# Kernel optimization log

Hardware: AMD Instinct MI355X
Metric: run time of the kernel (lower is better)

## Reference

```python
import jax, jax.numpy as jnp
import numpy as np

B, N, M, D = 4, 512, 512, 128
H, DOUT = 256, 128

def setup_inputs() -> dict:
    key = jax.random.key(0)
    k = jax.random.split(key, 4)
    X = jax.random.normal(k[0], (B, N, D), dtype=jnp.float32)
    Y = jax.random.normal(k[1], (B, M, D), dtype=jnp.float32)
    W1 = jax.random.normal(k[2], (2 * D, H), dtype=jnp.float32) / np.sqrt(2 * D)
    b1 = jnp.zeros((H,), dtype=jnp.float32)
    W2 = jax.random.normal(k[3], (H, DOUT), dtype=jnp.float32) / np.sqrt(H)
    b2 = jnp.zeros((DOUT,), dtype=jnp.float32)
    return {"X": X, "Y": Y, "W1": W1, "b1": b1, "W2": W2, "b2": b2}

def reference(X, Y, W1, b1, W2, b2):
    # pairs[b,n,m,:] = concat(Y[b,m], X[b,n])  -> [B,N,M,2D]
    n_ = X.shape[1]
    m_ = Y.shape[1]
    Ye = jnp.broadcast_to(Y[:, None, :, :], (X.shape[0], n_, m_, Y.shape[-1]))
    Xe = jnp.broadcast_to(X[:, :, None, :], (X.shape[0], n_, m_, X.shape[-1]))
    pairs = jnp.concatenate([Ye, Xe], axis=-1)
    # pointwise MLP: Linear -> ReLU -> Linear
    hdn = jax.nn.relu(jnp.einsum('bnmd,dh->bnmh', pairs, W1) + b1)
    Z = jnp.einsum('bnmh,ho->bnmo', hdn, W2) + b2
    # pool='sum' over the M (neighbor) dimension
    return jnp.sum(Z, axis=2)  # [B, N, DOUT]
```

## Files before the change

### kernel.cpp

```cpp
#include <hip/hip_runtime.h>

#define BB    4
#define NN    512
#define MM    512
#define DD    128
#define HH    256
#define DOUTC 128

typedef float v4f __attribute__((ext_vector_type(4)));

__global__ __launch_bounds__(1024) void precompute_ac(
    const float* __restrict__ X, const float* __restrict__ Y,
    const float* __restrict__ W1, const float* __restrict__ b1,
    float* __restrict__ AT, float* __restrict__ CT)
{
    __shared__ __align__(16) float rows[16][DD];
    __shared__ __align__(16) v4f mrg[3][4][4][64];
    const int bid = blockIdx.x;
    const int t   = threadIdx.x;
    const int isC = bid >> 7;
    const int r0  = (bid & 127) * 16;
    const float* src = isC ? X : Y;

    if (t < 512)
        reinterpret_cast<v4f*>(&rows[0][0])[t] =
            reinterpret_cast<const v4f*>(src + (size_t)r0 * DD)[t];
    __syncthreads();

    const int hq = t & 63;
    const int dq = (t >> 6) & 3;
    const int rs = t >> 8;
    const int d0 = dq * 32;
    const float* wp = W1 + (isC ? DD * HH : 0) + hq * 4;

    v4f acc[4];
#pragma unroll
    for (int r = 0; r < 4; ++r) acc[r] = (v4f){0.f, 0.f, 0.f, 0.f};

#pragma unroll 2
    for (int dg = 0; dg < 32; dg += 4) {
        const int d = d0 + dg;
        const v4f w0 = *reinterpret_cast<const v4f*>(&wp[(d + 0) * HH]);
        const v4f w1 = *reinterpret_cast<const v4f*>(&wp[(d + 1) * HH]);
        const v4f w2 = *reinterpret_cast<const v4f*>(&wp[(d + 2) * HH]);
        const v4f w3 = *reinterpret_cast<const v4f*>(&wp[(d + 3) * HH]);
#pragma unroll
        for (int r = 0; r < 4; ++r) {
            const v4f rv = *reinterpret_cast<const v4f*>(&rows[rs * 4 + r][d]);
            acc[r] += w0 * rv.x;
            acc[r] += w1 * rv.y;
            acc[r] += w2 * rv.z;
            acc[r] += w3 * rv.w;
        }
    }

    if (dq > 0) {
#pragma unroll
        for (int r = 0; r < 4; ++r) mrg[dq - 1][rs][r][hq] = acc[r];
    }
    __syncthreads();
    if (dq == 0) {
#pragma unroll
        for (int r = 0; r < 4; ++r) {
#pragma unroll
            for (int p = 0; p < 3; ++p) acc[r] += mrg[p][rs][r][hq];
        }
        v4f bias = (v4f){0.f, 0.f, 0.f, 0.f};
        if (isC) bias = *reinterpret_cast<const v4f*>(&b1[hq * 4]);
#pragma unroll
        for (int r = 0; r < 4; ++r) acc[r] += bias;

        const int grow = r0 + rs * 4;
        const int bb   = grow >> 9;
        const int mm   = grow & 511;
        float* Tb = isC ? CT : AT;
#pragma unroll
        for (int u = 0; u < 4; ++u) {
            const v4f w = (v4f){acc[0][u], acc[1][u], acc[2][u], acc[3][u]};
            *reinterpret_cast<v4f*>(
                &Tb[((size_t)(bb * HH + hq * 4 + u)) * 512 + mm]) = w;
        }
    }
}

__global__ __launch_bounds__(512) void sort_query(
    const float* __restrict__ AT, const float* __restrict__ CT,
    float* __restrict__ S)
{
    __shared__ float col[4][512];
    __shared__ float t1[4][512];
    __shared__ float t2[4][512];
    const int bid = blockIdx.x;
    const int b   = bid >> 6;
    const int h0  = (bid & 63) * 4;
    const int t   = threadIdx.x;

    const float* Abase = AT + ((size_t)(b * HH + h0)) * 512;
#pragma unroll
    for (int u = 0; u < 4; ++u)
        col[u][t] = Abase[(size_t)u * 512 + t];
    __syncthreads();

    for (int k = 2; k <= 512; k <<= 1) {
        for (int j = k >> 1; j > 0; j >>= 1) {
            const int p = t ^ j;
            if (p > t) {
                const bool asc = ((t & k) == 0);
#pragma unroll
                for (int u = 0; u < 4; ++u) {
                    const float x = col[u][t];
                    const float y = col[u][p];
                    if ((x > y) == asc) { col[u][t] = y; col[u][p] = x; }
                }
            }
            __syncthreads();
        }
    }

#pragma unroll
    for (int u = 0; u < 4; ++u)
        t1[u][t] = col[u][t] + ((t >= 1) ? col[u][t - 1] : 0.f);
    __syncthreads();
    {
        int d = 2;
#pragma unroll
        for (int s = 0; s < 8; ++s) {
            if ((s & 1) == 0) {
#pragma unroll
                for (int u = 0; u < 4; ++u)
                    t2[u][t] = t1[u][t] + ((t >= d) ? t1[u][t - d] : 0.f);
            } else {
#pragma unroll
                for (int u = 0; u < 4; ++u)
                    t1[u][t] = t2[u][t] + ((t >= d) ? t2[u][t - d] : 0.f);
            }
            __syncthreads();
            d <<= 1;
        }
    }

    const float* Cbase = CT + ((size_t)(b * HH + h0)) * 512;
    float cv[4], negc[4];
    int kk[4];
#pragma unroll
    for (int u = 0; u < 4; ++u) {
        cv[u]   = Cbase[(size_t)u * 512 + t];
        negc[u] = -cv[u];
        kk[u]   = 0;
    }
#pragma unroll
    for (int step = 512; step > 0; step >>= 1) {
#pragma unroll
        for (int u = 0; u < 4; ++u) {
            const int nk = kk[u] + step;
            if (nk <= 512 && col[u][nk - 1] < negc[u]) kk[u] = nk;
        }
    }

    v4f s4;
#pragma unroll
    for (int u = 0; u < 4; ++u) {
        const float T  = t1[u][511];
        const float Pk = (kk[u] > 0) ? t1[u][kk[u] - 1] : 0.f;
        s4[u] = (T - Pk) + (float)(512 - kk[u]) * cv[u];
    }
    *reinterpret_cast<v4f*>(&S[((size_t)(b * NN + t)) * HH + h0]) = s4;
}

__global__ __launch_bounds__(512) void epilogue(
    const float* __restrict__ S, const float* __restrict__ W2,
    const float* __restrict__ b2, float* __restrict__ out)
{
    __shared__ __align__(16) float Sl[4][HH];
    __shared__ __align__(16) v4f red[3 * 128];
    const int bn0 = blockIdx.x * 4;
    const int t   = threadIdx.x;

    if (t < 256)
        reinterpret_cast<v4f*>(&Sl[0][0])[t] =
            reinterpret_cast<const v4f*>(&S[(size_t)bn0 * HH])[t];
    __syncthreads();

    const int o0 = (t & 31) * 4;
    const int r  = (t >> 5) & 3;
    const int kq = t >> 7;
    const int k0 = kq * 64;
    v4f a4 = (v4f){0.f, 0.f, 0.f, 0.f};
    const float* w2p = W2 + o0;
#pragma unroll 4
    for (int k = k0; k < k0 + 64; k += 4) {
        const v4f sv = *reinterpret_cast<const v4f*>(&Sl[r][k]);
        const v4f wA = *reinterpret_cast<const v4f*>(&w2p[(k + 0) * DOUTC]);
        const v4f wB = *reinterpret_cast<const v4f*>(&w2p[(k + 1) * DOUTC]);
        const v4f wC = *reinterpret_cast<const v4f*>(&w2p[(k + 2) * DOUTC]);
        const v4f wD = *reinterpret_cast<const v4f*>(&w2p[(k + 3) * DOUTC]);
        a4 += wA * sv.x;
        a4 += wB * sv.y;
        a4 += wC * sv.z;
        a4 += wD * sv.w;
    }
    if (kq) red[(kq - 1) * 128 + (t & 127)] = a4;
    __syncthreads();
    if (kq == 0) {
#pragma unroll
        for (int p = 0; p < 3; ++p) a4 += red[p * 128 + (t & 127)];
        a4 += 512.f * (*reinterpret_cast<const v4f*>(&b2[o0]));
        *reinterpret_cast<v4f*>(&out[(size_t)(bn0 + r) * DOUTC + o0]) = a4;
    }
}

extern "C" void kernel_launch(void* const* d_in, const int* in_sizes, int n_in,
                              void* d_out, int out_size, void* d_ws, size_t ws_size,
                              hipStream_t stream) {
    const float* X  = (const float*)d_in[0];
    const float* Y  = (const float*)d_in[1];
    const float* W1 = (const float*)d_in[2];
    const float* b1 = (const float*)d_in[3];
    const float* W2 = (const float*)d_in[4];
    const float* b2 = (const float*)d_in[5];
    float* out = (float*)d_out;

    float* AT = (float*)d_ws;
    float* CT = AT + (size_t)BB * HH * 512;
    float* S  = CT + (size_t)BB * HH * 512;

    hipLaunchKernelGGL(precompute_ac, dim3(256), dim3(1024), 0, stream,
                       X, Y, W1, b1, AT, CT);
    hipLaunchKernelGGL(sort_query, dim3(256), dim3(512), 0, stream,
                       AT, CT, S);
    hipLaunchKernelGGL(epilogue, dim3(BB * NN / 4), dim3(512), 0, stream,
                       S, W2, b2, out);
}
```

Measured before the change: 45.01 us.

## Sort each column within one wavefront using registers and shuffles

After: 48.80 us. +8.4%, slower.

```diff
diff --git a/kernel.cpp b/kernel.cpp
--- a/kernel.cpp
+++ b/kernel.cpp
@@ -83,102 +83,110 @@
     }
 }
 
-__global__ __launch_bounds__(512) void sort_query(
+__global__ __launch_bounds__(256) void sort_query(
     const float* __restrict__ AT, const float* __restrict__ CT,
-    float* __restrict__ S)
+    float* __restrict__ ST)
 {
-    __shared__ float col[4][512];
-    __shared__ float t1[4][512];
-    __shared__ float t2[4][512];
-    const int bid = blockIdx.x;
-    const int b   = bid >> 6;
-    const int h0  = (bid & 63) * 4;
-    const int t   = threadIdx.x;
-
-    const float* Abase = AT + ((size_t)(b * HH + h0)) * 512;
-#pragma unroll
-    for (int u = 0; u < 4; ++u)
-        col[u][t] = Abase[(size_t)u * 512 + t];
-    __syncthreads();
+    __shared__ float vals[4][512];
+    __shared__ float pref[4][512];
+    const int wid = threadIdx.x >> 6;
+    const int l   = threadIdx.x & 63;
+    const int col = blockIdx.x * 4 + wid;
+
+    float a[8];
+    const float* Ac = AT + (size_t)col * 512;
+#pragma unroll
+    for (int r = 0; r < 8; ++r) a[r] = Ac[r * 64 + l];
 
     for (int k = 2; k <= 512; k <<= 1) {
         for (int j = k >> 1; j > 0; j >>= 1) {
-            const int p = t ^ j;
-            if (p > t) {
-                const bool asc = ((t & k) == 0);
-#pragma unroll
-                for (int u = 0; u < 4; ++u) {
-                    const float x = col[u][t];
-                    const float y = col[u][p];
-                    if ((x > y) == asc) { col[u][t] = y; col[u][p] = x; }
+            if (j >= 64) {
+                const int rj = j >> 6;
+#pragma unroll
+                for (int r = 0; r < 8; ++r) {
+                    if ((r & rj) == 0) {
+                        const int rh = r | rj;
+                        const bool asc = (((r << 6) & k) == 0);
+                        const float x = a[r], y = a[rh];
+                        const float mn = fminf(x, y), mx = fmaxf(x, y);
+                        a[r]  = asc ? mn : mx;
+                        a[rh] = asc ? mx : mn;
+                    }
+                }
+            } else {
+                const bool lower = ((l & j) == 0);
+#pragma unroll
+                for (int r = 0; r < 8; ++r) {
+                    const bool asc = (k >= 64) ? (((r << 6) & k) == 0)
+                                               : ((l & k) == 0);
+                    const float other = __shfl_xor(a[r], j, 64);
+                    const bool take_min = (lower == asc);
+                    const float mn = fminf(a[r], other);
+                    const float mx = fmaxf(a[r], other);
+                    a[r] = take_min ? mn : mx;
                 }
             }
-            __syncthreads();
-        }
-    }
-
-#pragma unroll
-    for (int u = 0; u < 4; ++u)
-        t1[u][t] = col[u][t] + ((t >= 1) ? col[u][t - 1] : 0.f);
-    __syncthreads();
-    {
-        int d = 2;
-#pragma unroll
-        for (int s = 0; s < 8; ++s) {
-            if ((s & 1) == 0) {
-#pragma unroll
-                for (int u = 0; u < 4; ++u)
-                    t2[u][t] = t1[u][t] + ((t >= d) ? t1[u][t - d] : 0.f);
-            } else {
-#pragma unroll
-                for (int u = 0; u < 4; ++u)
-                    t1[u][t] = t2[u][t] + ((t >= d) ? t2[u][t - d] : 0.f);
-            }
-            __syncthreads();
-            d <<= 1;
-        }
-    }
-
-    const float* Cbase = CT + ((size_t)(b * HH + h0)) * 512;
-    float cv[4], negc[4];
-    int kk[4];
-#pragma unroll
-    for (int u = 0; u < 4; ++u) {
-        cv[u]   = Cbase[(size_t)u * 512 + t];
-        negc[u] = -cv[u];
-        kk[u]   = 0;
-    }
-#pragma unroll
-    for (int step = 512; step > 0; step >>= 1) {
-#pragma unroll
-        for (int u = 0; u < 4; ++u) {
-            const int nk = kk[u] + step;
-            if (nk <= 512 && col[u][nk - 1] < negc[u]) kk[u] = nk;
-        }
-    }
-
-    v4f s4;
-#pragma unroll
-    for (int u = 0; u < 4; ++u) {
-        const float T  = t1[u][511];
-        const float Pk = (kk[u] > 0) ? t1[u][kk[u] - 1] : 0.f;
-        s4[u] = (T - Pk) + (float)(512 - kk[u]) * cv[u];
-    }
-    *reinterpret_cast<v4f*>(&S[((size_t)(b * NN + t)) * HH + h0]) = s4;
+        }
+    }
+
+#pragma unroll
+    for (int r = 0; r < 8; ++r) vals[wid][r * 64 + l] = a[r];
+    asm volatile("s_waitcnt lgkmcnt(0)" ::: "memory");
+    __builtin_amdgcn_sched_barrier(0);
+
+    float v[8], p[8];
+#pragma unroll
+    for (int q = 0; q < 8; ++q) v[q] = vals[wid][l * 8 + q];
+    p[0] = v[0];
+#pragma unroll
+    for (int q = 1; q < 8; ++q) p[q] = p[q - 1] + v[q];
+    float run = p[7];
+#pragma unroll
+    for (int off = 1; off < 64; off <<= 1) {
+        const float tv = __shfl_up(run, off, 64);
+        if (l >= off) run += tv;
+    }
+    const float Ttot = __shfl(run, 63, 64);
+    const float excl = run - p[7];
+#pragma unroll
+    for (int q = 0; q < 8; ++q) pref[wid][l * 8 + q] = p[q] + excl;
+    asm volatile("s_waitcnt lgkmcnt(0)" ::: "memory");
+    __builtin_amdgcn_sched_barrier(0);
+
+    const float* Cc = CT + (size_t)col * 512;
+    float* Sc       = ST + (size_t)col * 512;
+#pragma unroll 2
+    for (int q = 0; q < 8; ++q) {
+        const int n = q * 64 + l;
+        const float c = Cc[n];
+        const float negc = -c;
+        int kk = 0;
+#pragma unroll
+        for (int step = 512; step > 0; step >>= 1) {
+            const int nk = kk + step;
+            if (nk <= 512 && vals[wid][nk - 1] < negc) kk = nk;
+        }
+        const float Pk = (kk > 0) ? pref[wid][kk - 1] : 0.f;
+        Sc[n] = (Ttot - Pk) + (float)(512 - kk) * c;
+    }
 }
 
 __global__ __launch_bounds__(512) void epilogue(
-    const float* __restrict__ S, const float* __restrict__ W2,
+    const float* __restrict__ ST, const float* __restrict__ W2,
     const float* __restrict__ b2, float* __restrict__ out)
 {
     __shared__ __align__(16) float Sl[4][HH];
     __shared__ __align__(16) v4f red[3 * 128];
     const int bn0 = blockIdx.x * 4;
+    const int b   = bn0 >> 9;
+    const int n0l = bn0 & 511;
     const int t   = threadIdx.x;
 
-    if (t < 256)
-        reinterpret_cast<v4f*>(&Sl[0][0])[t] =
-            reinterpret_cast<const v4f*>(&S[(size_t)bn0 * HH])[t];
+    if (t < 256) {
+#pragma unroll
+        for (int r = 0; r < 4; ++r)
+            Sl[r][t] = ST[((size_t)(b * HH + t)) * 512 + n0l + r];
+    }
     __syncthreads();
 
     const int o0 = (t & 31) * 4;
@@ -222,12 +230,12 @@
 
     float* AT = (float*)d_ws;
     float* CT = AT + (size_t)BB * HH * 512;
-    float* S  = CT + (size_t)BB * HH * 512;
+    float* ST = CT + (size_t)BB * HH * 512;
 
     hipLaunchKernelGGL(precompute_ac, dim3(256), dim3(1024), 0, stream,
                        X, Y, W1, b1, AT, CT);
-    hipLaunchKernelGGL(sort_query, dim3(256), dim3(512), 0, stream,
-                       AT, CT, S);
+    hipLaunchKernelGGL(sort_query, dim3(256), dim3(256), 0, stream,
+                       AT, CT, ST);
     hipLaunchKernelGGL(epilogue, dim3(BB * NN / 4), dim3(512), 0, stream,
-                       S, W2, b2, out);
-}
+                       ST, W2, b2, out);
+}
```
